# Performance work log

Measured on AMD Instinct MI355X. Metric: run time of the kernel, lower is better.

Reference implementation:

```python
import jax, jax.numpy as jnp
import numpy as np

B, T, D_MODEL, HEAD_SIZE = 8, 1024, 1024, 64
BLOCK_SIZE = 1024  # == max_relative_pos


def setup_inputs() -> dict:
    key = jax.random.key(0)
    ks = jax.random.split(key, 7)
    s = 1.0 / np.sqrt(D_MODEL)
    return {
        "x": jax.random.normal(ks[0], (B, T, D_MODEL), dtype=jnp.float32),
        "Wk": jax.random.normal(ks[1], (D_MODEL, HEAD_SIZE), dtype=jnp.float32) * s,
        "bk": jax.random.normal(ks[2], (HEAD_SIZE,), dtype=jnp.float32) * 0.02,
        "Wq": jax.random.normal(ks[3], (D_MODEL, HEAD_SIZE), dtype=jnp.float32) * s,
        "bq": jax.random.normal(ks[4], (HEAD_SIZE,), dtype=jnp.float32) * 0.02,
        "Wv": jax.random.normal(ks[5], (D_MODEL, HEAD_SIZE), dtype=jnp.float32) * s,
        "rel_emb": jax.random.normal(ks[6], (2 * BLOCK_SIZE + 1, HEAD_SIZE), dtype=jnp.float32) * 0.02,
        "mask": 1,
    }


def reference(x, Wk, bk, Wq, bq, Wv, rel_emb, mask):
    Bb, Tt, _ = x.shape
    hs = Wk.shape[1]
    max_rel = (rel_emb.shape[0] - 1) // 2

    k = x @ Wk + bk          # [B,T,hs]
    q = x @ Wq + bq          # [B,T,hs]
    v = x @ Wv               # [B,T,hs]

    pos = jnp.arange(Tt)
    idx = jnp.clip(pos[:, None] - pos[None, :], -max_rel, max_rel) + max_rel
    r = rel_emb[idx]         # [T,T,hs], r[i,j] = emb(clip(i-j))

    # scores[b,i,j] = (q[b,i] + r[i,j]) . (k[b,j] + r[j,i]) / sqrt(hs)
    scale = 1.0 / np.sqrt(hs).astype(np.float32)
    scores = (
        jnp.einsum("bid,bjd->bij", q, k)
        + jnp.einsum("bid,jid->bij", q, r)   # q_i . r[j,i]
        + jnp.einsum("ijd,bjd->bij", r, k)   # r[i,j] . k_j
        + jnp.einsum("ijd,jid->ij", r, r)[None]  # r[i,j] . r[j,i]
    ) * scale

    if mask:  # static Python int -> causal mask, matches tril masked_fill
        causal = jnp.tril(jnp.ones((Tt, Tt), dtype=bool))
        scores = jnp.where(causal, scores, jnp.float32(-jnp.inf))

    w = jax.nn.softmax(scores, axis=-1)  # dropout is identity in eval mode
    return w @ v  # [B,T,hs]
```

## Files before the change

### kernel.cpp

```cpp
#include <hip/hip_runtime.h>
#include <hip/hip_bf16.h>
#include <math.h>


typedef __hip_bfloat16 bf16;
typedef __attribute__((ext_vector_type(8))) short short8;
typedef __attribute__((ext_vector_type(4))) float f32x4;

#define NTRI 136
#define MFMA16(a, b, c) __builtin_amdgcn_mfma_f32_16x16x32_bf16(a, b, c, 0, 0, 0)

__device__ __forceinline__ float bf2f(bf16 h) { return __bfloat162float(h); }
__device__ __forceinline__ bf16 f2bf(float f) { return __float2bfloat16(f); }
__device__ __forceinline__ short bfs(float f) {
  bf16 h = __float2bfloat16(f);
  return *(short*)&h;
}

union U16 {
  uint4 u;
  short8 s;
};
__device__ __forceinline__ short8 ldfrag(const bf16* p) {
  U16 x;
  x.u = *(const uint4*)p;
  return x.s;
}

__global__ __launch_bounds__(256) void prep_kernel(
    const float* __restrict__ Wk, const float* __restrict__ Wq, const float* __restrict__ Wv,
    const float* __restrict__ E, bf16* __restrict__ WT, bf16* __restrict__ Ep,
    bf16* __restrict__ Erev, float* __restrict__ rrG) {
  const int bid = blockIdx.x, t = threadIdx.x;
  if (bid < 768) {
    int idx = bid * 256 + t;
    int sel = idx >> 16, r = idx & 65535;
    int n = r >> 10, kk = r & 1023;
    const float* W = (sel == 0) ? Wk : (sel == 1) ? Wq : Wv;
    WT[idx] = f2bf(W[kk * 64 + n]);
  } else if (bid < 1281) {
    int idx = (bid - 768) * 256 + t;
    if (idx < 2049 * 64) {
      int tt = idx >> 6, d = idx & 63;
      Ep[idx] = f2bf(E[idx]);
      Erev[idx] = f2bf(E[(2048 - tt) * 64 + d]);
    }
  } else {
    int dlt = ((bid - 1281) << 2) + (t >> 6);
    int d = t & 63;
    float p = E[(size_t)(1024 + dlt) * 64 + d] * E[(size_t)(1024 - dlt) * 64 + d];
#pragma unroll
    for (int off = 32; off > 0; off >>= 1) p += __shfl_down(p, off);
    if (d == 0) rrG[64 + dlt] = p;
  }
}

__global__ __launch_bounds__(256, 2) void qkv_mfma(
    const float* __restrict__ x, const bf16* __restrict__ WT,
    const float* __restrict__ bk, const float* __restrict__ bq,
    bf16* __restrict__ qB, bf16* __restrict__ kB, bf16* __restrict__ vT) {
  const int R0 = blockIdx.x << 4;
  const int t = threadIdx.x;
  const int lane = t & 63, wave = t >> 6;
  const int m = lane & 15, quad = lane >> 4;

  __shared__ float RED[4][16][196];
  __shared__ bf16 VTS[64][24];

  const float* xrow = x + (size_t)(R0 + m) * 1024 + (wave << 8);
  f32x4 acc[3][4];
#pragma unroll
  for (int s = 0; s < 3; ++s)
#pragma unroll
    for (int c = 0; c < 4; ++c) acc[s][c] = (f32x4){0.f, 0.f, 0.f, 0.f};

#pragma unroll
  for (int ks = 0; ks < 8; ++ks) {
    const int k0 = ks * 32 + quad * 8;
    float4 xa = *(const float4*)(xrow + k0);
    float4 xb = *(const float4*)(xrow + k0 + 4);
    short8 a;
    a[0] = bfs(xa.x); a[1] = bfs(xa.y); a[2] = bfs(xa.z); a[3] = bfs(xa.w);
    a[4] = bfs(xb.x); a[5] = bfs(xb.y); a[6] = bfs(xb.z); a[7] = bfs(xb.w);
    const int kg = (wave << 8) + k0;
#pragma unroll
    for (int sel = 0; sel < 3; ++sel)
#pragma unroll
      for (int ct = 0; ct < 4; ++ct) {
        const bf16* bb = WT + ((size_t)(sel * 64 + ct * 16 + m) << 10) + kg;
        acc[sel][ct] = MFMA16(a, ldfrag(bb), acc[sel][ct]);
      }
  }

#pragma unroll
  for (int sel = 0; sel < 3; ++sel)
#pragma unroll
    for (int ct = 0; ct < 4; ++ct)
#pragma unroll
      for (int r = 0; r < 4; ++r)
        RED[wave][quad * 4 + r][sel * 64 + ct * 16 + m] = acc[sel][ct][r];
  __syncthreads();

#pragma unroll
  for (int e = 0; e < 12; ++e) {
    int idx = e * 256 + t;
    int row = idx / 192, c = idx - row * 192;
    float s = RED[0][row][c] + RED[1][row][c] + RED[2][row][c] + RED[3][row][c];
    int sel = c >> 6, col = c & 63;
    size_t grow = (size_t)(R0 + row);
    if (sel == 0) kB[grow * 64 + col] = f2bf(s + bk[col]);
    else if (sel == 1) qB[grow * 64 + col] = f2bf(s + bq[col]);
    else VTS[col][row] = f2bf(s);
  }
  __syncthreads();
  {
    int dd = t >> 2, h = (t & 3) << 2;
    int b = R0 >> 10, tloc = R0 & 1023;
    *(uint2*)(vT + ((size_t)((b << 6) + dd) << 10) + tloc + h) = *(const uint2*)&VTS[dd][h];
  }
}

__global__ __launch_bounds__(256, 3) void flash_mfma(
    const bf16* __restrict__ qB, const bf16* __restrict__ kB, const bf16* __restrict__ vT,
    const bf16* __restrict__ Ep, const bf16* __restrict__ Erev, const float* __restrict__ rrG,
    float* __restrict__ Oacc, float* __restrict__ Lacc) {
  const int bx = blockIdx.x;
  const int b = bx / NTRI;
  const int rr_ = bx - b * NTRI;
  int it = (int)((sqrtf(8.f * rr_ + 1.f) - 1.f) * 0.5f);
  while ((it + 1) * (it + 2) / 2 <= rr_) ++it;
  while (it * (it + 1) / 2 > rr_) --it;
  const int jt = rr_ - it * (it + 1) / 2;
  const int I0 = it << 6, J0 = jt << 6;
  const int D = I0 - J0, w0 = D - 64;

  const int t = threadIdx.x;
  const int lane = t & 63, wave = t >> 6;
  const int m = lane & 15, quad = lane >> 4;
  const int strip = wave << 4;

  __shared__ __align__(16) bf16 M2S[64][136];
  __shared__ bf16 M3S[64][136];
  bf16 (*PS)[80] = (bf16(*)[80])M2S;

  const bf16* qbase = qB + ((size_t)((b << 10) + I0 + strip + m) << 6);
  const short8 aq0 = ldfrag(qbase + quad * 8);
  const short8 aq1 = ldfrag(qbase + 32 + quad * 8);
  const bf16* kbase = kB + ((size_t)((b << 10) + J0 + strip + m) << 6);
  const short8 ak0 = ldfrag(kbase + quad * 8);
  const short8 ak1 = ldfrag(kbase + 32 + quad * 8);

  const bf16* erb = Erev + ((size_t)(1024 + w0) << 6);
#pragma unroll
  for (int ct = 0; ct < 8; ++ct) {
    const bf16* bb = erb + ((size_t)(ct * 16 + m) << 6) + quad * 8;
    const float rv = rrG[64 + w0 + ct * 16 + m];
    f32x4 c = (f32x4){0.f, 0.f, 0.f, 0.f};
    c = MFMA16(aq0, ldfrag(bb), c);
    c = MFMA16(aq1, ldfrag(bb + 32), c);
#pragma unroll
    for (int r = 0; r < 4; ++r) M2S[strip + quad * 4 + r][ct * 16 + m] = f2bf(c[r] + rv);
  }
  const bf16* epb = Ep + ((size_t)(1024 + w0) << 6);
#pragma unroll
  for (int ct = 0; ct < 8; ++ct) {
    const bf16* bb = epb + ((size_t)(ct * 16 + m) << 6) + quad * 8;
    f32x4 c = (f32x4){0.f, 0.f, 0.f, 0.f};
    c = MFMA16(ak0, ldfrag(bb), c);
    c = MFMA16(ak1, ldfrag(bb + 32), c);
#pragma unroll
    for (int r = 0; r < 4; ++r) M3S[strip + quad * 4 + r][ct * 16 + m] = f2bf(c[r]);
  }
  f32x4 acc[4];
#pragma unroll
  for (int ct = 0; ct < 4; ++ct) {
    const bf16* bb = kB + ((size_t)((b << 10) + J0 + ct * 16 + m) << 6) + quad * 8;
    f32x4 c = (f32x4){0.f, 0.f, 0.f, 0.f};
    c = MFMA16(aq0, ldfrag(bb), c);
    c = MFMA16(aq1, ldfrag(bb + 32), c);
    acc[ct] = c;
  }
  __syncthreads();

  float sc[4][4], lrow[4] = {0.f, 0.f, 0.f, 0.f};
#pragma unroll
  for (int ct = 0; ct < 4; ++ct) {
    const int uj = ct * 16 + m;
#pragma unroll
    for (int r = 0; r < 4; ++r) {
      const int ui = strip + quad * 4 + r;
      float s;
      if (ui - uj + D >= 0) {
        const int wi = ui - uj + 64;
        s = (acc[ct][r] + bf2f(M2S[ui][wi]) + bf2f(M3S[uj][wi])) * 0.125f;
      } else {
        s = -INFINITY;
      }
      float p = __expf(s - 8.0f);
      sc[ct][r] = p;
      lrow[r] += p;
    }
  }
#pragma unroll
  for (int r = 0; r < 4; ++r) {
#pragma unroll
    for (int off = 1; off < 16; off <<= 1) lrow[r] += __shfl_xor(lrow[r], off);
  }
  if (m == 0) {
#pragma unroll
    for (int r = 0; r < 4; ++r)
      atomicAdd(&Lacc[(b << 10) + I0 + strip + quad * 4 + r], lrow[r]);
  }
  __syncthreads();
#pragma unroll
  for (int ct = 0; ct < 4; ++ct)
#pragma unroll
    for (int r = 0; r < 4; ++r) PS[strip + quad * 4 + r][ct * 16 + m] = f2bf(sc[ct][r]);
  __syncthreads();

  const short8 ap0 = ldfrag(&PS[strip + m][quad * 8]);
  const short8 ap1 = ldfrag(&PS[strip + m][32 + quad * 8]);
  float* ob = Oacc + ((size_t)((b << 10) + I0) << 6);
#pragma unroll
  for (int ct = 0; ct < 4; ++ct) {
    const bf16* bb = vT + ((size_t)(b * 64 + ct * 16 + m) << 10) + J0 + quad * 8;
    f32x4 o = (f32x4){0.f, 0.f, 0.f, 0.f};
    o = MFMA16(ap0, ldfrag(bb), o);
    o = MFMA16(ap1, ldfrag(bb + 32), o);
#pragma unroll
    for (int r = 0; r < 4; ++r)
      atomicAdd(&ob[(size_t)(strip + quad * 4 + r) * 64 + ct * 16 + m], o[r]);
  }
}

__global__ __launch_bounds__(256) void normalize_kernel(
    const float* __restrict__ Oacc, const float* __restrict__ Lacc, float* __restrict__ out) {
  int idx = blockIdx.x * 256 + threadIdx.x;
  out[idx] = Oacc[idx] / Lacc[idx >> 6];
}

extern "C" void kernel_launch(void* const* d_in, const int* in_sizes, int n_in,
                              void* d_out, int out_size, void* d_ws, size_t ws_size,
                              hipStream_t stream) {
  const float* x = (const float*)d_in[0];
  const float* Wk = (const float*)d_in[1];
  const float* bk = (const float*)d_in[2];
  const float* Wq = (const float*)d_in[3];
  const float* bq = (const float*)d_in[4];
  const float* Wv = (const float*)d_in[5];
  const float* E = (const float*)d_in[6];
  float* out = (float*)d_out;

  float* wsf = (float*)d_ws;
  float* Oacc = wsf;
  float* Lacc = wsf + 524288;
  float* rrG = wsf + 532480;
  bf16* qB = (bf16*)(rrG + 1152);
  bf16* kB = qB + 524288;
  bf16* vT = kB + 524288;
  bf16* Ep = vT + 524288;
  bf16* Erev = Ep + 131200;
  bf16* WT = Erev + 131200;

  hipMemsetAsync(Oacc, 0, (524288 + 8192) * sizeof(float), stream);
  prep_kernel<<<1537, 256, 0, stream>>>(Wk, Wq, Wv, E, WT, Ep, Erev, rrG);
  qkv_mfma<<<512, 256, 0, stream>>>(x, WT, bk, bq, qB, kB, vT);
  flash_mfma<<<8 * NTRI, 256, 0, stream>>>(qB, kB, vT, Ep, Erev, rrG, Oacc, Lacc);
  normalize_kernel<<<2048, 256, 0, stream>>>(Oacc, Lacc, out);
}
```

Measured before the change: 150.5 us.

## Fuse all stages into one persistent cooperative kernel with grid syncs

Replaces the memset plus four separate launches with a single cooperative persistent kernel that runs the prep, QKV projection, flash tiles and normalization as grid-strided phases separated by grid.sync. The goal is to remove per-launch overhead and the inter-kernel gaps, which weigh heavily at this small runtime. In exchange it adds grid-wide barriers, limits the grid to occupancy×256 workgroups and assumes 256 CUs, and keeps a fallback to the old multi-launch path if the cooperative launch fails.

```diff
diff --git a/kernel.cpp b/kernel.cpp
--- a/kernel.cpp
+++ b/kernel.cpp
@@ -1,7 +1,10 @@
 #include <hip/hip_runtime.h>
+#include <hip/hip_cooperative_groups.h>
 #include <hip/hip_bf16.h>
 #include <math.h>
 
+
+namespace cg = cooperative_groups;
 
 typedef __hip_bfloat16 bf16;
 typedef __attribute__((ext_vector_type(8))) short short8;
@@ -25,6 +28,235 @@
   U16 x;
   x.u = *(const uint4*)p;
   return x.s;
+}
+
+struct QkvShared {
+  float RED[4][16][194];
+  bf16 VTS[64][24];
+};
+struct FlashShared {
+  __align__(16) bf16 M2S[64][136];
+  bf16 M3S[64][136];
+};
+
+__device__ __forceinline__ void qkv_unit(
+    int R0, int t, const float* __restrict__ x, const bf16* __restrict__ WT,
+    const float* __restrict__ bk, const float* __restrict__ bq,
+    bf16* __restrict__ qB, bf16* __restrict__ kB, bf16* __restrict__ vT, QkvShared& S) {
+  const int lane = t & 63, wave = t >> 6;
+  const int m = lane & 15, quad = lane >> 4;
+
+  const float* xrow = x + (size_t)(R0 + m) * 1024 + (wave << 8);
+  f32x4 acc[3][4];
+#pragma unroll
+  for (int s = 0; s < 3; ++s)
+#pragma unroll
+    for (int c = 0; c < 4; ++c) acc[s][c] = (f32x4){0.f, 0.f, 0.f, 0.f};
+
+#pragma unroll
+  for (int ks = 0; ks < 8; ++ks) {
+    const int k0 = ks * 32 + quad * 8;
+    float4 xa = *(const float4*)(xrow + k0);
+    float4 xb = *(const float4*)(xrow + k0 + 4);
+    short8 a;
+    a[0] = bfs(xa.x); a[1] = bfs(xa.y); a[2] = bfs(xa.z); a[3] = bfs(xa.w);
+    a[4] = bfs(xb.x); a[5] = bfs(xb.y); a[6] = bfs(xb.z); a[7] = bfs(xb.w);
+    const int kg = (wave << 8) + k0;
+#pragma unroll
+    for (int sel = 0; sel < 3; ++sel)
+#pragma unroll
+      for (int ct = 0; ct < 4; ++ct) {
+        const bf16* bb = WT + ((size_t)(sel * 64 + ct * 16 + m) << 10) + kg;
+        acc[sel][ct] = MFMA16(a, ldfrag(bb), acc[sel][ct]);
+      }
+  }
+
+#pragma unroll
+  for (int sel = 0; sel < 3; ++sel)
+#pragma unroll
+    for (int ct = 0; ct < 4; ++ct)
+#pragma unroll
+      for (int r = 0; r < 4; ++r)
+        S.RED[wave][quad * 4 + r][sel * 64 + ct * 16 + m] = acc[sel][ct][r];
+  __syncthreads();
+
+#pragma unroll
+  for (int e = 0; e < 12; ++e) {
+    int idx = e * 256 + t;
+    int row = idx / 192, c = idx - row * 192;
+    float s = S.RED[0][row][c] + S.RED[1][row][c] + S.RED[2][row][c] + S.RED[3][row][c];
+    int sel = c >> 6, col = c & 63;
+    size_t grow = (size_t)(R0 + row);
+    if (sel == 0) kB[grow * 64 + col] = f2bf(s + bk[col]);
+    else if (sel == 1) qB[grow * 64 + col] = f2bf(s + bq[col]);
+    else S.VTS[col][row] = f2bf(s);
+  }
+  __syncthreads();
+  {
+    int dd = t >> 2, h = (t & 3) << 2;
+    int b = R0 >> 10, tloc = R0 & 1023;
+    *(uint2*)(vT + ((size_t)((b << 6) + dd) << 10) + tloc + h) = *(const uint2*)&S.VTS[dd][h];
+  }
+  __syncthreads();
+}
+
+__device__ __forceinline__ void flash_unit(
+    int u, int t, const bf16* __restrict__ qB, const bf16* __restrict__ kB,
+    const bf16* __restrict__ vT, const bf16* __restrict__ Ep, const bf16* __restrict__ Erev,
+    const float* __restrict__ rrG, float* __restrict__ Oacc, float* __restrict__ Lacc,
+    FlashShared& S) {
+  const int b = u / NTRI;
+  const int rr_ = u - b * NTRI;
+  int it = (int)((sqrtf(8.f * rr_ + 1.f) - 1.f) * 0.5f);
+  while ((it + 1) * (it + 2) / 2 <= rr_) ++it;
+  while (it * (it + 1) / 2 > rr_) --it;
+  const int jt = rr_ - it * (it + 1) / 2;
+  const int I0 = it << 6, J0 = jt << 6;
+  const int D = I0 - J0, w0 = D - 64;
+
+  const int lane = t & 63, wave = t >> 6;
+  const int m = lane & 15, quad = lane >> 4;
+  const int strip = wave << 4;
+
+  bf16 (*PS)[80] = (bf16(*)[80])S.M2S;
+
+  const bf16* qbase = qB + ((size_t)((b << 10) + I0 + strip + m) << 6);
+  const short8 aq0 = ldfrag(qbase + quad * 8);
+  const short8 aq1 = ldfrag(qbase + 32 + quad * 8);
+  const bf16* kbase = kB + ((size_t)((b << 10) + J0 + strip + m) << 6);
+  const short8 ak0 = ldfrag(kbase + quad * 8);
+  const short8 ak1 = ldfrag(kbase + 32 + quad * 8);
+
+  const bf16* erb = Erev + ((size_t)(1024 + w0) << 6);
+#pragma unroll
+  for (int ct = 0; ct < 8; ++ct) {
+    const bf16* bb = erb + ((size_t)(ct * 16 + m) << 6) + quad * 8;
+    const float rv = rrG[64 + w0 + ct * 16 + m];
+    f32x4 c = (f32x4){0.f, 0.f, 0.f, 0.f};
+    c = MFMA16(aq0, ldfrag(bb), c);
+    c = MFMA16(aq1, ldfrag(bb + 32), c);
+#pragma unroll
+    for (int r = 0; r < 4; ++r) S.M2S[strip + quad * 4 + r][ct * 16 + m] = f2bf(c[r] + rv);
+  }
+  const bf16* epb = Ep + ((size_t)(1024 + w0) << 6);
+#pragma unroll
+  for (int ct = 0; ct < 8; ++ct) {
+    const bf16* bb = epb + ((size_t)(ct * 16 + m) << 6) + quad * 8;
+    f32x4 c = (f32x4){0.f, 0.f, 0.f, 0.f};
+    c = MFMA16(ak0, ldfrag(bb), c);
+    c = MFMA16(ak1, ldfrag(bb + 32), c);
+#pragma unroll
+    for (int r = 0; r < 4; ++r) S.M3S[strip + quad * 4 + r][ct * 16 + m] = f2bf(c[r]);
+  }
+  f32x4 acc[4];
+#pragma unroll
+  for (int ct = 0; ct < 4; ++ct) {
+    const bf16* bb = kB + ((size_t)((b << 10) + J0 + ct * 16 + m) << 6) + quad * 8;
+    f32x4 c = (f32x4){0.f, 0.f, 0.f, 0.f};
+    c = MFMA16(aq0, ldfrag(bb), c);
+    c = MFMA16(aq1, ldfrag(bb + 32), c);
+    acc[ct] = c;
+  }
+  __syncthreads();
+
+  float sc[4][4], lrow[4] = {0.f, 0.f, 0.f, 0.f};
+#pragma unroll
+  for (int ct = 0; ct < 4; ++ct) {
+    const int uj = ct * 16 + m;
+#pragma unroll
+    for (int r = 0; r < 4; ++r) {
+      const int ui = strip + quad * 4 + r;
+      float s;
+      if (ui - uj + D >= 0) {
+        const int wi = ui - uj + 64;
+        s = (acc[ct][r] + bf2f(S.M2S[ui][wi]) + bf2f(S.M3S[uj][wi])) * 0.125f;
+      } else {
+        s = -INFINITY;
+      }
+      float p = __expf(s - 8.0f);
+      sc[ct][r] = p;
+      lrow[r] += p;
+    }
+  }
+#pragma unroll
+  for (int r = 0; r < 4; ++r) {
+#pragma unroll
+    for (int off = 1; off < 16; off <<= 1) lrow[r] += __shfl_xor(lrow[r], off);
+  }
+  if (m == 0) {
+#pragma unroll
+    for (int r = 0; r < 4; ++r)
+      atomicAdd(&Lacc[(b << 10) + I0 + strip + quad * 4 + r], lrow[r]);
+  }
+  __syncthreads();
+#pragma unroll
+  for (int ct = 0; ct < 4; ++ct)
+#pragma unroll
+    for (int r = 0; r < 4; ++r) PS[strip + quad * 4 + r][ct * 16 + m] = f2bf(sc[ct][r]);
+  __syncthreads();
+
+  const short8 ap0 = ldfrag(&PS[strip + m][quad * 8]);
+  const short8 ap1 = ldfrag(&PS[strip + m][32 + quad * 8]);
+  float* ob = Oacc + ((size_t)((b << 10) + I0) << 6);
+#pragma unroll
+  for (int ct = 0; ct < 4; ++ct) {
+    const bf16* bb = vT + ((size_t)(b * 64 + ct * 16 + m) << 10) + J0 + quad * 8;
+    f32x4 o = (f32x4){0.f, 0.f, 0.f, 0.f};
+    o = MFMA16(ap0, ldfrag(bb), o);
+    o = MFMA16(ap1, ldfrag(bb + 32), o);
+#pragma unroll
+    for (int r = 0; r < 4; ++r)
+      atomicAdd(&ob[(size_t)(strip + quad * 4 + r) * 64 + ct * 16 + m], o[r]);
+  }
+  __syncthreads();
+}
+
+struct MegaArgs {
+  const float *x, *Wk, *bk, *Wq, *bq, *Wv, *E;
+  float *out, *Oacc, *Lacc, *rrG;
+  bf16 *qB, *kB, *vT, *Ep, *Erev, *WT;
+};
+
+__global__ __launch_bounds__(256, 3) void mega_kernel(MegaArgs A) {
+  __shared__ union {
+    QkvShared q;
+    FlashShared f;
+  } sh;
+  cg::grid_group grid = cg::this_grid();
+  const int bx = blockIdx.x, t = threadIdx.x;
+  const int nwg = gridDim.x;
+  const int tid = bx * 256 + t, tot = nwg * 256;
+
+  for (int i = tid; i < 196608; i += tot) {
+    int sel = i >> 16, r = i & 65535;
+    int n = r >> 10, kk = r & 1023;
+    const float* W = (sel == 0) ? A.Wk : (sel == 1) ? A.Wq : A.Wv;
+    A.WT[i] = f2bf(W[kk * 64 + n]);
+  }
+  for (int i = tid; i < 2049 * 64; i += tot) {
+    int tt = i >> 6, d = i & 63;
+    A.Ep[i] = f2bf(A.E[i]);
+    A.Erev[i] = f2bf(A.E[(size_t)(2048 - tt) * 64 + d]);
+  }
+  for (int i = tid; i < 532480; i += tot) A.Oacc[i] = 0.f;
+  for (int w = (bx << 2) + (t >> 6); w < 1024; w += (nwg << 2)) {
+    int d = t & 63;
+    float p = A.E[(size_t)(1024 + w) * 64 + d] * A.E[(size_t)(1024 - w) * 64 + d];
+#pragma unroll
+    for (int off = 32; off > 0; off >>= 1) p += __shfl_down(p, off);
+    if (d == 0) A.rrG[64 + w] = p;
+  }
+  grid.sync();
+
+  for (int unit = bx; unit < 512; unit += nwg)
+    qkv_unit(unit << 4, t, A.x, A.WT, A.bk, A.bq, A.qB, A.kB, A.vT, sh.q);
+  grid.sync();
+
+  for (int u = bx; u < 8 * NTRI; u += nwg)
+    flash_unit(u, t, A.qB, A.kB, A.vT, A.Ep, A.Erev, A.rrG, A.Oacc, A.Lacc, sh.f);
+  grid.sync();
+
+  for (int i = tid; i < 524288; i += tot) A.out[i] = A.Oacc[i] / A.Lacc[i >> 6];
 }
 
 __global__ __launch_bounds__(256) void prep_kernel(
@@ -43,7 +275,7 @@
     if (idx < 2049 * 64) {
       int tt = idx >> 6, d = idx & 63;
       Ep[idx] = f2bf(E[idx]);
-      Erev[idx] = f2bf(E[(2048 - tt) * 64 + d]);
+      Erev[idx] = f2bf(E[(size_t)(2048 - tt) * 64 + d]);
     }
   } else {
     int dlt = ((bid - 1281) << 2) + (t >> 6);
@@ -59,178 +291,16 @@
     const float* __restrict__ x, const bf16* __restrict__ WT,
     const float* __restrict__ bk, const float* __restrict__ bq,
     bf16* __restrict__ qB, bf16* __restrict__ kB, bf16* __restrict__ vT) {
-  const int R0 = blockIdx.x << 4;
-  const int t = threadIdx.x;
-  const int lane = t & 63, wave = t >> 6;
-  const int m = lane & 15, quad = lane >> 4;
-
-  __shared__ float RED[4][16][196];
-  __shared__ bf16 VTS[64][24];
-
-  const float* xrow = x + (size_t)(R0 + m) * 1024 + (wave << 8);
-  f32x4 acc[3][4];
-#pragma unroll
-  for (int s = 0; s < 3; ++s)
-#pragma unroll
-    for (int c = 0; c < 4; ++c) acc[s][c] = (f32x4){0.f, 0.f, 0.f, 0.f};
-
-#pragma unroll
-  for (int ks = 0; ks < 8; ++ks) {
-    const int k0 = ks * 32 + quad * 8;
-    float4 xa = *(const float4*)(xrow + k0);
-    float4 xb = *(const float4*)(xrow + k0 + 4);
-    short8 a;
-    a[0] = bfs(xa.x); a[1] = bfs(xa.y); a[2] = bfs(xa.z); a[3] = bfs(xa.w);
-    a[4] = bfs(xb.x); a[5] = bfs(xb.y); a[6] = bfs(xb.z); a[7] = bfs(xb.w);
-    const int kg = (wave << 8) + k0;
-#pragma unroll
-    for (int sel = 0; sel < 3; ++sel)
-#pragma unroll
-      for (int ct = 0; ct < 4; ++ct) {
-        const bf16* bb = WT + ((size_t)(sel * 64 + ct * 16 + m) << 10) + kg;
-        acc[sel][ct] = MFMA16(a, ldfrag(bb), acc[sel][ct]);
-      }
-  }
-
-#pragma unroll
-  for (int sel = 0; sel < 3; ++sel)
-#pragma unroll
-    for (int ct = 0; ct < 4; ++ct)
-#pragma unroll
-      for (int r = 0; r < 4; ++r)
-        RED[wave][quad * 4 + r][sel * 64 + ct * 16 + m] = acc[sel][ct][r];
-  __syncthreads();
-
-#pragma unroll
-  for (int e = 0; e < 12; ++e) {
-    int idx = e * 256 + t;
-    int row = idx / 192, c = idx - row * 192;
-    float s = RED[0][row][c] + RED[1][row][c] + RED[2][row][c] + RED[3][row][c];
-    int sel = c >> 6, col = c & 63;
-    size_t grow = (size_t)(R0 + row);
-    if (sel == 0) kB[grow * 64 + col] = f2bf(s + bk[col]);
-    else if (sel == 1) qB[grow * 64 + col] = f2bf(s + bq[col]);
-    else VTS[col][row] = f2bf(s);
-  }
-  __syncthreads();
-  {
-    int dd = t >> 2, h = (t & 3) << 2;
-    int b = R0 >> 10, tloc = R0 & 1023;
-    *(uint2*)(vT + ((size_t)((b << 6) + dd) << 10) + tloc + h) = *(const uint2*)&VTS[dd][h];
-  }
+  __shared__ QkvShared S;
+  qkv_unit(blockIdx.x << 4, threadIdx.x, x, WT, bk, bq, qB, kB, vT, S);
 }
 
 __global__ __launch_bounds__(256, 3) void flash_mfma(
     const bf16* __restrict__ qB, const bf16* __restrict__ kB, const bf16* __restrict__ vT,
     const bf16* __restrict__ Ep, const bf16* __restrict__ Erev, const float* __restrict__ rrG,
     float* __restrict__ Oacc, float* __restrict__ Lacc) {
-  const int bx = blockIdx.x;
-  const int b = bx / NTRI;
-  const int rr_ = bx - b * NTRI;
-  int it = (int)((sqrtf(8.f * rr_ + 1.f) - 1.f) * 0.5f);
-  while ((it + 1) * (it + 2) / 2 <= rr_) ++it;
-  while (it * (it + 1) / 2 > rr_) --it;
-  const int jt = rr_ - it * (it + 1) / 2;
-  const int I0 = it << 6, J0 = jt << 6;
-  const int D = I0 - J0, w0 = D - 64;
-
-  const int t = threadIdx.x;
-  const int lane = t & 63, wave = t >> 6;
-  const int m = lane & 15, quad = lane >> 4;
-  const int strip = wave << 4;
-
-  __shared__ __align__(16) bf16 M2S[64][136];
-  __shared__ bf16 M3S[64][136];
-  bf16 (*PS)[80] = (bf16(*)[80])M2S;
-
-  const bf16* qbase = qB + ((size_t)((b << 10) + I0 + strip + m) << 6);
-  const short8 aq0 = ldfrag(qbase + quad * 8);
-  const short8 aq1 = ldfrag(qbase + 32 + quad * 8);
-  const bf16* kbase = kB + ((size_t)((b << 10) + J0 + strip + m) << 6);
-  const short8 ak0 = ldfrag(kbase + quad * 8);
-  const short8 ak1 = ldfrag(kbase + 32 + quad * 8);
-
-  const bf16* erb = Erev + ((size_t)(1024 + w0) << 6);
-#pragma unroll
-  for (int ct = 0; ct < 8; ++ct) {
-    const bf16* bb = erb + ((size_t)(ct * 16 + m) << 6) + quad * 8;
-    const float rv = rrG[64 + w0 + ct * 16 + m];
-    f32x4 c = (f32x4){0.f, 0.f, 0.f, 0.f};
-    c = MFMA16(aq0, ldfrag(bb), c);
-    c = MFMA16(aq1, ldfrag(bb + 32), c);
-#pragma unroll
-    for (int r = 0; r < 4; ++r) M2S[strip + quad * 4 + r][ct * 16 + m] = f2bf(c[r] + rv);
-  }
-  const bf16* epb = Ep + ((size_t)(1024 + w0) << 6);
-#pragma unroll
-  for (int ct = 0; ct < 8; ++ct) {
-    const bf16* bb = epb + ((size_t)(ct * 16 + m) << 6) + quad * 8;
-    f32x4 c = (f32x4){0.f, 0.f, 0.f, 0.f};
-    c = MFMA16(ak0, ldfrag(bb), c);
-    c = MFMA16(ak1, ldfrag(bb + 32), c);
-#pragma unroll
-    for (int r = 0; r < 4; ++r) M3S[strip + quad * 4 + r][ct * 16 + m] = f2bf(c[r]);
-  }
-  f32x4 acc[4];
-#pragma unroll
-  for (int ct = 0; ct < 4; ++ct) {
-    const bf16* bb = kB + ((size_t)((b << 10) + J0 + ct * 16 + m) << 6) + quad * 8;
-    f32x4 c = (f32x4){0.f, 0.f, 0.f, 0.f};
-    c = MFMA16(aq0, ldfrag(bb), c);
-    c = MFMA16(aq1, ldfrag(bb + 32), c);
-    acc[ct] = c;
-  }
-  __syncthreads();
-
-  float sc[4][4], lrow[4] = {0.f, 0.f, 0.f, 0.f};
-#pragma unroll
-  for (int ct = 0; ct < 4; ++ct) {
-    const int uj = ct * 16 + m;
-#pragma unroll
-    for (int r = 0; r < 4; ++r) {
-      const int ui = strip + quad * 4 + r;
-      float s;
-      if (ui - uj + D >= 0) {
-        const int wi = ui - uj + 64;
-        s = (acc[ct][r] + bf2f(M2S[ui][wi]) + bf2f(M3S[uj][wi])) * 0.125f;
-      } else {
-        s = -INFINITY;
-      }
-      float p = __expf(s - 8.0f);
-      sc[ct][r] = p;
-      lrow[r] += p;
-    }
-  }
-#pragma unroll
-  for (int r = 0; r < 4; ++r) {
-#pragma unroll
-    for (int off = 1; off < 16; off <<= 1) lrow[r] += __shfl_xor(lrow[r], off);
-  }
-  if (m == 0) {
-#pragma unroll
-    for (int r = 0; r < 4; ++r)
-      atomicAdd(&Lacc[(b << 10) + I0 + strip + quad * 4 + r], lrow[r]);
-  }
-  __syncthreads();
-#pragma unroll
-  for (int ct = 0; ct < 4; ++ct)
-#pragma unroll
-    for (int r = 0; r < 4; ++r) PS[strip + quad * 4 + r][ct * 16 + m] = f2bf(sc[ct][r]);
-  __syncthreads();
-
-  const short8 ap0 = ldfrag(&PS[strip + m][quad * 8]);
-  const short8 ap1 = ldfrag(&PS[strip + m][32 + quad * 8]);
-  float* ob = Oacc + ((size_t)((b << 10) + I0) << 6);
-#pragma unroll
-  for (int ct = 0; ct < 4; ++ct) {
-    const bf16* bb = vT + ((size_t)(b * 64 + ct * 16 + m) << 10) + J0 + quad * 8;
-    f32x4 o = (f32x4){0.f, 0.f, 0.f, 0.f};
-    o = MFMA16(ap0, ldfrag(bb), o);
-    o = MFMA16(ap1, ldfrag(bb + 32), o);
-#pragma unroll
-    for (int r = 0; r < 4; ++r)
-      atomicAdd(&ob[(size_t)(strip + quad * 4 + r) * 64 + ct * 16 + m], o[r]);
-  }
+  __shared__ FlashShared S;
+  flash_unit(blockIdx.x, threadIdx.x, qB, kB, vT, Ep, Erev, rrG, Oacc, Lacc, S);
 }
 
 __global__ __launch_bounds__(256) void normalize_kernel(
@@ -262,9 +332,22 @@
   bf16* Erev = Ep + 131200;
   bf16* WT = Erev + 131200;
 
-  hipMemsetAsync(Oacc, 0, (524288 + 8192) * sizeof(float), stream);
-  prep_kernel<<<1537, 256, 0, stream>>>(Wk, Wq, Wv, E, WT, Ep, Erev, rrG);
-  qkv_mfma<<<512, 256, 0, stream>>>(x, WT, bk, bq, qB, kB, vT);
-  flash_mfma<<<8 * NTRI, 256, 0, stream>>>(qB, kB, vT, Ep, Erev, rrG, Oacc, Lacc);
-  normalize_kernel<<<2048, 256, 0, stream>>>(Oacc, Lacc, out);
-}
+  MegaArgs A = {x, Wk, bk, Wq, bq, Wv, E, out, Oacc, Lacc, rrG, qB, kB, vT, Ep, Erev, WT};
+
+  int occ = 0;
+  hipError_t qe = hipOccupancyMaxActiveBlocksPerMultiprocessor(&occ, mega_kernel, 256, 0);
+  if (occ > 3) occ = 3;
+
+  hipError_t le = hipErrorUnknown;
+  if (qe == hipSuccess && occ >= 1) {
+    void* params[] = {(void*)&A};
+    le = hipLaunchCooperativeKernel(mega_kernel, dim3(occ * 256), dim3(256), params, 0, stream);
+  }
+  if (le != hipSuccess) {
+    hipMemsetAsync(Oacc, 0, (524288 + 8192) * sizeof(float), stream);
+    prep_kernel<<<1537, 256, 0, stream>>>(Wk, Wq, Wv, E, WT, Ep, Erev, rrG);
+    qkv_mfma<<<512, 256, 0, stream>>>(x, WT, bk, bq, qB, kB, vT);
+    flash_mfma<<<8 * NTRI, 256, 0, stream>>>(qB, kB, vT, Ep, Erev, rrG, Oacc, Lacc);
+    normalize_kernel<<<2048, 256, 0, stream>>>(Oacc, Lacc, out);
+  }
+}
```

Result: slower. 314.5 us (+109.0%).

## Fuse zeroing into prep and normalization into flash via last-block counter

Applied to the files above, without the earlier changes.

Replaces the separate memset with extra zeroing blocks in the prep kernel, and removes the normalize kernel by having the last tile block per query row-block (detected with an atomic counter) divide the accumulated output by the row sums. This cuts two launches and one full pass over the accumulator. It adds a counter atomic and a serialized tail of work in whichever block finishes last for each row-block, and depends on acquire/release ordering being correct for the atomically accumulated data.

```diff
diff --git a/kernel.cpp b/kernel.cpp
--- a/kernel.cpp
+++ b/kernel.cpp
@@ -30,7 +30,7 @@
 __global__ __launch_bounds__(256) void prep_kernel(
     const float* __restrict__ Wk, const float* __restrict__ Wq, const float* __restrict__ Wv,
     const float* __restrict__ E, bf16* __restrict__ WT, bf16* __restrict__ Ep,
-    bf16* __restrict__ Erev, float* __restrict__ rrG) {
+    bf16* __restrict__ Erev, float* __restrict__ rrG, float* __restrict__ zeroBase) {
   const int bid = blockIdx.x, t = threadIdx.x;
   if (bid < 768) {
     int idx = bid * 256 + t;
@@ -43,15 +43,19 @@
     if (idx < 2049 * 64) {
       int tt = idx >> 6, d = idx & 63;
       Ep[idx] = f2bf(E[idx]);
-      Erev[idx] = f2bf(E[(2048 - tt) * 64 + d]);
+      Erev[idx] = f2bf(E[(size_t)(2048 - tt) * 64 + d]);
     }
-  } else {
+  } else if (bid < 1537) {
     int dlt = ((bid - 1281) << 2) + (t >> 6);
     int d = t & 63;
     float p = E[(size_t)(1024 + dlt) * 64 + d] * E[(size_t)(1024 - dlt) * 64 + d];
 #pragma unroll
     for (int off = 32; off > 0; off >>= 1) p += __shfl_down(p, off);
     if (d == 0) rrG[64 + dlt] = p;
+  } else {
+    int idx4 = (bid - 1537) * 256 + t;
+    if (idx4 * 4 < 532608)
+      *(float4*)(zeroBase + idx4 * 4) = make_float4(0.f, 0.f, 0.f, 0.f);
   }
 }
 
@@ -123,7 +127,8 @@
 __global__ __launch_bounds__(256, 3) void flash_mfma(
     const bf16* __restrict__ qB, const bf16* __restrict__ kB, const bf16* __restrict__ vT,
     const bf16* __restrict__ Ep, const bf16* __restrict__ Erev, const float* __restrict__ rrG,
-    float* __restrict__ Oacc, float* __restrict__ Lacc) {
+    float* __restrict__ Oacc, float* __restrict__ Lacc, int* __restrict__ cnt,
+    float* __restrict__ out) {
   const int bx = blockIdx.x;
   const int b = bx / NTRI;
   const int rr_ = bx - b * NTRI;
@@ -141,6 +146,8 @@
 
   __shared__ __align__(16) bf16 M2S[64][136];
   __shared__ bf16 M3S[64][136];
+  __shared__ int lastFlag;
+  __shared__ float shL[64];
   bf16 (*PS)[80] = (bf16(*)[80])M2S;
 
   const bf16* qbase = qB + ((size_t)((b << 10) + I0 + strip + m) << 6);
@@ -231,12 +238,28 @@
     for (int r = 0; r < 4; ++r)
       atomicAdd(&ob[(size_t)(strip + quad * 4 + r) * 64 + ct * 16 + m], o[r]);
   }
-}
-
-__global__ __launch_bounds__(256) void normalize_kernel(
-    const float* __restrict__ Oacc, const float* __restrict__ Lacc, float* __restrict__ out) {
-  int idx = blockIdx.x * 256 + threadIdx.x;
-  out[idx] = Oacc[idx] / Lacc[idx >> 6];
+
+  __syncthreads();
+  if (t == 0) {
+    int old = __hip_atomic_fetch_add(&cnt[(b << 4) + it], 1, __ATOMIC_ACQ_REL,
+                                     __HIP_MEMORY_SCOPE_AGENT);
+    lastFlag = (old == it);
+  }
+  __syncthreads();
+  if (lastFlag) {
+    if (t < 64)
+      shL[t] = __hip_atomic_load(&Lacc[(b << 10) + I0 + t], __ATOMIC_RELAXED,
+                                 __HIP_MEMORY_SCOPE_AGENT);
+    __syncthreads();
+    const size_t base = ((size_t)((b << 10) + I0)) << 6;
+#pragma unroll
+    for (int u = 0; u < 16; ++u) {
+      int idx = u * 256 + t;
+      float v = __hip_atomic_load(&Oacc[base + idx], __ATOMIC_RELAXED,
+                                  __HIP_MEMORY_SCOPE_AGENT);
+      out[base + idx] = v / shL[idx >> 6];
+    }
+  }
 }
 
 extern "C" void kernel_launch(void* const* d_in, const int* in_sizes, int n_in,
@@ -254,7 +277,8 @@
   float* wsf = (float*)d_ws;
   float* Oacc = wsf;
   float* Lacc = wsf + 524288;
-  float* rrG = wsf + 532480;
+  int* cnt = (int*)(wsf + 532480);
+  float* rrG = wsf + 532608;
   bf16* qB = (bf16*)(rrG + 1152);
   bf16* kB = qB + 524288;
   bf16* vT = kB + 524288;
@@ -262,9 +286,7 @@
   bf16* Erev = Ep + 131200;
   bf16* WT = Erev + 131200;
 
-  hipMemsetAsync(Oacc, 0, (524288 + 8192) * sizeof(float), stream);
-  prep_kernel<<<1537, 256, 0, stream>>>(Wk, Wq, Wv, E, WT, Ep, Erev, rrG);
+  prep_kernel<<<2058, 256, 0, stream>>>(Wk, Wq, Wv, E, WT, Ep, Erev, rrG, Oacc);
   qkv_mfma<<<512, 256, 0, stream>>>(x, WT, bk, bq, qB, kB, vT);
-  flash_mfma<<<8 * NTRI, 256, 0, stream>>>(qB, kB, vT, Ep, Erev, rrG, Oacc, Lacc);
-  normalize_kernel<<<2048, 256, 0, stream>>>(Oacc, Lacc, out);
-}
+  flash_mfma<<<8 * NTRI, 256, 0, stream>>>(qB, kB, vT, Ep, Erev, rrG, Oacc, Lacc, cnt, out);
+}
```

Measured after the change: 175.2 us. 1.16x slower.

## Fold accumulator zeroing into prep kernel and interleave relative-embedding MFMAs

Applied to the files above, without the earlier changes.

Drops the separate hipMemsetAsync and zeroes the Oacc/Lacc accumulators in extra blocks of the prep kernel, removing one launch. In the flash kernel the two relative-embedding projection loops are merged so the Erev and Ep fragment loads are issued together, which exposes more memory-level parallelism. The flash kernel's launch bound is lowered from 3 to 2 blocks per SM, giving the compiler more registers for the extra live fragments at the cost of occupancy.

```diff
diff --git a/kernel.cpp b/kernel.cpp
--- a/kernel.cpp
+++ b/kernel.cpp
@@ -30,7 +30,7 @@
 __global__ __launch_bounds__(256) void prep_kernel(
     const float* __restrict__ Wk, const float* __restrict__ Wq, const float* __restrict__ Wv,
     const float* __restrict__ E, bf16* __restrict__ WT, bf16* __restrict__ Ep,
-    bf16* __restrict__ Erev, float* __restrict__ rrG) {
+    bf16* __restrict__ Erev, float* __restrict__ rrG, float* __restrict__ zeroBase) {
   const int bid = blockIdx.x, t = threadIdx.x;
   if (bid < 768) {
     int idx = bid * 256 + t;
@@ -43,15 +43,19 @@
     if (idx < 2049 * 64) {
       int tt = idx >> 6, d = idx & 63;
       Ep[idx] = f2bf(E[idx]);
-      Erev[idx] = f2bf(E[(2048 - tt) * 64 + d]);
+      Erev[idx] = f2bf(E[(size_t)(2048 - tt) * 64 + d]);
     }
-  } else {
+  } else if (bid < 1537) {
     int dlt = ((bid - 1281) << 2) + (t >> 6);
     int d = t & 63;
     float p = E[(size_t)(1024 + dlt) * 64 + d] * E[(size_t)(1024 - dlt) * 64 + d];
 #pragma unroll
     for (int off = 32; off > 0; off >>= 1) p += __shfl_down(p, off);
     if (d == 0) rrG[64 + dlt] = p;
+  } else {
+    int idx4 = (bid - 1537) * 256 + t;
+    if (idx4 * 4 < 532480)
+      *(float4*)(zeroBase + idx4 * 4) = make_float4(0.f, 0.f, 0.f, 0.f);
   }
 }
 
@@ -120,7 +124,7 @@
   }
 }
 
-__global__ __launch_bounds__(256, 3) void flash_mfma(
+__global__ __launch_bounds__(256, 2) void flash_mfma(
     const bf16* __restrict__ qB, const bf16* __restrict__ kB, const bf16* __restrict__ vT,
     const bf16* __restrict__ Ep, const bf16* __restrict__ Erev, const float* __restrict__ rrG,
     float* __restrict__ Oacc, float* __restrict__ Lacc) {
@@ -151,25 +155,27 @@
   const short8 ak1 = ldfrag(kbase + 32 + quad * 8);
 
   const bf16* erb = Erev + ((size_t)(1024 + w0) << 6);
+  const bf16* epb = Ep + ((size_t)(1024 + w0) << 6);
 #pragma unroll
   for (int ct = 0; ct < 8; ++ct) {
-    const bf16* bb = erb + ((size_t)(ct * 16 + m) << 6) + quad * 8;
+    const bf16* bb2 = erb + ((size_t)(ct * 16 + m) << 6) + quad * 8;
+    const bf16* bb3 = epb + ((size_t)(ct * 16 + m) << 6) + quad * 8;
+    const short8 b20 = ldfrag(bb2);
+    const short8 b21 = ldfrag(bb2 + 32);
+    const short8 b30 = ldfrag(bb3);
+    const short8 b31 = ldfrag(bb3 + 32);
     const float rv = rrG[64 + w0 + ct * 16 + m];
-    f32x4 c = (f32x4){0.f, 0.f, 0.f, 0.f};
-    c = MFMA16(aq0, ldfrag(bb), c);
-    c = MFMA16(aq1, ldfrag(bb + 32), c);
-#pragma unroll
-    for (int r = 0; r < 4; ++r) M2S[strip + quad * 4 + r][ct * 16 + m] = f2bf(c[r] + rv);
-  }
-  const bf16* epb = Ep + ((size_t)(1024 + w0) << 6);
-#pragma unroll
-  for (int ct = 0; ct < 8; ++ct) {
-    const bf16* bb = epb + ((size_t)(ct * 16 + m) << 6) + quad * 8;
-    f32x4 c = (f32x4){0.f, 0.f, 0.f, 0.f};
-    c = MFMA16(ak0, ldfrag(bb), c);
-    c = MFMA16(ak1, ldfrag(bb + 32), c);
-#pragma unroll
-    for (int r = 0; r < 4; ++r) M3S[strip + quad * 4 + r][ct * 16 + m] = f2bf(c[r]);
+    f32x4 c2 = (f32x4){0.f, 0.f, 0.f, 0.f};
+    c2 = MFMA16(aq0, b20, c2);
+    c2 = MFMA16(aq1, b21, c2);
+    f32x4 c3 = (f32x4){0.f, 0.f, 0.f, 0.f};
+    c3 = MFMA16(ak0, b30, c3);
+    c3 = MFMA16(ak1, b31, c3);
+#pragma unroll
+    for (int r = 0; r < 4; ++r) {
+      M2S[strip + quad * 4 + r][ct * 16 + m] = f2bf(c2[r] + rv);
+      M3S[strip + quad * 4 + r][ct * 16 + m] = f2bf(c3[r]);
+    }
   }
   f32x4 acc[4];
 #pragma unroll
@@ -262,8 +268,7 @@
   bf16* Erev = Ep + 131200;
   bf16* WT = Erev + 131200;
 
-  hipMemsetAsync(Oacc, 0, (524288 + 8192) * sizeof(float), stream);
-  prep_kernel<<<1537, 256, 0, stream>>>(Wk, Wq, Wv, E, WT, Ep, Erev, rrG);
+  prep_kernel<<<2058, 256, 0, stream>>>(Wk, Wq, Wv, E, WT, Ep, Erev, rrG, Oacc);
   qkv_mfma<<<512, 256, 0, stream>>>(x, WT, bk, bq, qB, kB, vT);
   flash_mfma<<<8 * NTRI, 256, 0, stream>>>(qB, kB, vT, Ep, Erev, rrG, Oacc, Lacc);
   normalize_kernel<<<2048, 256, 0, stream>>>(Oacc, Lacc, out);
```

After: 147.6 us. About the same (-1.9%).
